# Kernel optimization log

Hardware: AMD Instinct MI355X
Metric: run time of the kernel (lower is better)

## Reference

```python
import jax, jax.numpy as jnp
import numpy as np

HEADS = 16
TOPK = 2048  # dsa_topk


def setup_inputs() -> dict:
    key = jax.random.key(0)
    ks = jax.random.split(key, 9)
    B, Q, KV, C = 2, 2048, 16384, 1024
    w = lambda k: jax.random.normal(k, (C, C), dtype=jnp.float32) * 0.02
    return {
        "hidden_states": jax.random.normal(ks[0], (B, Q, C), dtype=jnp.float32),
        "encoder_hidden_states": jax.random.normal(ks[1], (B, KV, C), dtype=jnp.float32),
        "Wq": w(ks[2]),
        "Wk": w(ks[3]),
        "Wv": w(ks[4]),
        "Wo": w(ks[5]),
        "bo": jnp.zeros((C,), dtype=jnp.float32),
        "Wg": jax.random.normal(ks[6], (C, C), dtype=jnp.float32) * 0.01,  # xavier gain 0.1
        "bg": jnp.full((C,), -1.5, dtype=jnp.float32),  # gate_init_bias
    }


def reference(hidden_states, encoder_hidden_states, Wq, Wk, Wv, Wo, bo, Wg, bg):
    B, Q, C = hidden_states.shape
    H = HEADS
    D = C // H
    scale = 1.0 / jnp.sqrt(jnp.asarray(D, dtype=hidden_states.dtype))

    # projections -> [B, H, S, D]
    q = (hidden_states @ Wq).reshape(B, Q, H, D).transpose(0, 2, 1, 3)
    k = (encoder_hidden_states @ Wk).reshape(B, -1, H, D).transpose(0, 2, 1, 3)
    v = (encoder_hidden_states @ Wv).reshape(B, -1, H, D).transpose(0, 2, 1, 3)

    # _sparse_select: query-summary scored top-k KV gather (kv_len > TOPK here)
    q_summary = q.mean(axis=2)                                   # [B, H, D]
    sel_score = jnp.einsum("bhd,bhkd->bhk", q_summary, k) * scale
    idx = jax.lax.top_k(sel_score, TOPK)[1]                      # [B, H, TOPK]
    k_sel = jnp.take_along_axis(k, idx[..., None], axis=2)       # [B, H, TOPK, D]
    v_sel = jnp.take_along_axis(v, idx[..., None], axis=2)

    # attention over selected KV
    scores = jnp.einsum("bhqd,bhkd->bhqk", q, k_sel) * scale
    probs = jax.nn.softmax(scores.astype(jnp.float32), axis=-1).astype(scores.dtype)
    out = jnp.einsum("bhqk,bhkd->bhqd", probs, v_sel)
    out = out.transpose(0, 2, 1, 3).reshape(B, Q, C)

    # sigmoid gate + output projection (to_out[1] dropout is identity at eval)
    out = out * jax.nn.sigmoid(out @ Wg + bg)
    out = out @ Wo + bo

    # residual_connection=True, rescale_output_factor=1.0
    return out + hidden_states
```

## Files before the change

### kernel.cpp

```cpp
#include <hip/hip_runtime.h>
#include <hip/hip_bf16.h>

typedef unsigned short u16;
typedef __bf16 bf16x8 __attribute__((ext_vector_type(8)));
typedef float f32x4 __attribute__((ext_vector_type(4)));

__device__ __forceinline__ u16 f2bf(float f) {
    union { float f; unsigned int u; } v; v.f = f;
    unsigned int u = v.u;
    unsigned int r = (u + 0x7fffu + ((u >> 16) & 1u)) >> 16;
    return (u16)r;
}
__device__ __forceinline__ float bf2f(u16 b) {
    union { unsigned int u; float f; } v; v.u = ((unsigned int)b) << 16;
    return v.f;
}

__device__ __forceinline__ void glds16(const u16* g, u16* l) {
    __builtin_amdgcn_global_load_lds(
        (__attribute__((address_space(1))) void*)(g),
        (__attribute__((address_space(3))) void*)(l), 16, 0, 0);
}

__global__ __launch_bounds__(256) void cast_bf16_kernel(const float* __restrict__ src,
                                                        u16* __restrict__ dst, int n4) {
    int i = blockIdx.x * 256 + threadIdx.x;
    if (i >= n4) return;
    float4 v = ((const float4*)src)[i];
    ushort4 o;
    o.x = f2bf(v.x); o.y = f2bf(v.y); o.z = f2bf(v.z); o.w = f2bf(v.w);
    ((ushort4*)dst)[i] = o;
}

__global__ __launch_bounds__(256) void transpose_cast_kernel(
    const float* __restrict__ Wq, const float* __restrict__ Wk, const float* __restrict__ Wv,
    const float* __restrict__ Wg, const float* __restrict__ Wo,
    u16* __restrict__ WqT, u16* __restrict__ WkvT, u16* __restrict__ WgT, u16* __restrict__ WoT) {
    __shared__ float tile[32][33];
    const float* src; u16* dst;
    switch (blockIdx.z) {
        case 0: src = Wq; dst = WqT; break;
        case 1: src = Wk; dst = WkvT; break;
        case 2: src = Wv; dst = WkvT + (size_t)1024 * 1024; break;
        case 3: src = Wg; dst = WgT; break;
        default: src = Wo; dst = WoT; break;
    }
    int n0 = blockIdx.x * 32, k0 = blockIdx.y * 32;
    int tx = threadIdx.x, ty = threadIdx.y;
    #pragma unroll
    for (int j = 0; j < 4; j++)
        tile[ty + j * 8][tx] = src[(size_t)(k0 + ty + j * 8) * 1024 + n0 + tx];
    __syncthreads();
    #pragma unroll
    for (int j = 0; j < 4; j++)
        dst[(size_t)(n0 + ty + j * 8) * 1024 + k0 + tx] = f2bf(tile[tx][ty + j * 8]);
}

template <int EPI>
__global__ __launch_bounds__(256) void gemm_bf16(
    const u16* __restrict__ A, const u16* __restrict__ B, int ldc,
    u16* __restrict__ Cbf, const float* __restrict__ bias,
    const u16* __restrict__ mul_src, const float* __restrict__ add_src,
    float* __restrict__ Cf) {
    constexpr int K = 1024;
    const int tid = threadIdx.x;
    const int w = tid >> 6, l = tid & 63;
    const int lr = l & 15, lg = l >> 4;
    const int wr = w >> 1, wc = w & 1;
    const int m0 = blockIdx.y * 128, n0 = blockIdx.x * 128;

    __shared__ u16 As[128 * 64];
    __shared__ u16 Bs[128 * 64];

    const f32x4 fz = {0.f, 0.f, 0.f, 0.f};
    f32x4 acc[4][4];
    #pragma unroll
    for (int i = 0; i < 4; i++)
        #pragma unroll
        for (int j = 0; j < 4; j++) acc[i][j] = fz;

    const int lane_row = l >> 3;
    const int lane_sl  = l & 7;
    const int src_ch   = lane_sl ^ lane_row;
    const u16* Ab = A + (size_t)(m0 + w * 32 + lane_row) * K + src_ch * 8;
    const u16* Bb = B + (size_t)(n0 + w * 32 + lane_row) * K + src_ch * 8;

    for (int kt = 0; kt < K; kt += 64) {
        __syncthreads();
        #pragma unroll
        for (int j = 0; j < 4; j++) {
            glds16(Ab + (size_t)j * 8 * K + kt, As + (w * 32 + j * 8) * 64);
            glds16(Bb + (size_t)j * 8 * K + kt, Bs + (w * 32 + j * 8) * 64);
        }
        __syncthreads();
        #pragma unroll
        for (int kk = 0; kk < 2; kk++) {
            bf16x8 af[4], bfr[4];
            #pragma unroll
            for (int mi = 0; mi < 4; mi++) {
                int row = wr * 64 + mi * 16 + lr;
                int ch = (kk * 4 + lg) ^ (row & 7);
                af[mi] = *(const bf16x8*)(As + row * 64 + ch * 8);
            }
            #pragma unroll
            for (int ni = 0; ni < 4; ni++) {
                int row = wc * 64 + ni * 16 + lr;
                int ch = (kk * 4 + lg) ^ (row & 7);
                bfr[ni] = *(const bf16x8*)(Bs + row * 64 + ch * 8);
            }
            #pragma unroll
            for (int mi = 0; mi < 4; mi++)
                #pragma unroll
                for (int ni = 0; ni < 4; ni++)
                    acc[mi][ni] = __builtin_amdgcn_mfma_f32_16x16x32_bf16(
                        af[mi], bfr[ni], acc[mi][ni], 0, 0, 0);
        }
    }

    #pragma unroll
    for (int mi = 0; mi < 4; mi++) {
        #pragma unroll
        for (int ni = 0; ni < 4; ni++) {
            #pragma unroll
            for (int r = 0; r < 4; r++) {
                int gm = m0 + wr * 64 + mi * 16 + lg * 4 + r;
                int gn = n0 + wc * 64 + ni * 16 + lr;
                float v = acc[mi][ni][r];
                if (EPI == 0) {
                    Cbf[(size_t)gm * ldc + gn] = f2bf(v);
                } else if (EPI == 2) {
                    float g = v + bias[gn];
                    float a = bf2f(mul_src[(size_t)gm * ldc + gn]);
                    float sg = 1.f / (1.f + __expf(-g));
                    Cbf[(size_t)gm * ldc + gn] = f2bf(a * sg);
                } else {
                    Cf[(size_t)gm * ldc + gn] = v + bias[gn] + add_src[(size_t)gm * ldc + gn];
                }
            }
        }
    }
}

__global__ __launch_bounds__(256) void hsum1_kernel(const float* __restrict__ hidden,
                                                    float* __restrict__ part) {
    int b = blockIdx.x, chunk = blockIdx.y;
    int tid = threadIdx.x;
    const float4* src = (const float4*)(hidden + ((size_t)b * 2048 + chunk * 16) * 1024) + tid;
    float4 acc = {0.f, 0.f, 0.f, 0.f};
    #pragma unroll
    for (int r = 0; r < 16; r++) {
        float4 v = src[r * 256];
        acc.x += v.x; acc.y += v.y; acc.z += v.z; acc.w += v.w;
    }
    ((float4*)(part + ((size_t)b * 128 + chunk) * 1024))[tid] = acc;
}

__global__ __launch_bounds__(256) void hsum2_kernel(const float* __restrict__ part,
                                                    float* __restrict__ hm) {
    int b = blockIdx.x, tid = threadIdx.x;
    const float4* src = (const float4*)(part + (size_t)b * 128 * 1024) + tid;
    float4 acc = {0.f, 0.f, 0.f, 0.f};
    for (int c = 0; c < 128; c++) {
        float4 v = src[c * 256];
        acc.x += v.x; acc.y += v.y; acc.z += v.z; acc.w += v.w;
    }
    const float inv = 1.f / 2048.f;
    acc.x *= inv; acc.y *= inv; acc.z *= inv; acc.w *= inv;
    ((float4*)(hm + (size_t)b * 1024))[tid] = acc;
}

__global__ __launch_bounds__(256) void qz_kernel(const float* __restrict__ hm,
                                                 const u16* __restrict__ WqT,
                                                 const u16* __restrict__ WkT,
                                                 u16* __restrict__ z_bf) {
    int bh = blockIdx.x, b = bh >> 4, h = bh & 15;
    int tid = threadIdx.x;
    __shared__ float hm_l[1024];
    __shared__ float qs_l[64];
    __shared__ float red[256];
    ((float4*)hm_l)[tid] = ((const float4*)(hm + (size_t)b * 1024))[tid];
    __syncthreads();
    {
        int d = tid >> 2, q = tid & 3;
        const u16* wq = WqT + (size_t)(h * 64 + d) * 1024 + q * 256;
        float a = 0.f;
        for (int i = 0; i < 256; i += 8) {
            uint4 u = *(const uint4*)(wq + i);
            const u16* p = (const u16*)&u;
            #pragma unroll
            for (int j = 0; j < 8; j++) a += bf2f(p[j]) * hm_l[q * 256 + i + j];
        }
        red[tid] = a;
    }
    __syncthreads();
    if (tid < 64)
        qs_l[tid] = red[tid * 4] + red[tid * 4 + 1] + red[tid * 4 + 2] + red[tid * 4 + 3];
    __syncthreads();
    {
        float z0 = 0.f, z1 = 0.f, z2 = 0.f, z3 = 0.f;
        for (int d = 0; d < 64; d++) {
            float qs = qs_l[d];
            const u16* wk = WkT + (size_t)(h * 64 + d) * 1024 + tid * 4;
            uint2 u = *(const uint2*)wk;
            const u16* p = (const u16*)&u;
            z0 += qs * bf2f(p[0]); z1 += qs * bf2f(p[1]);
            z2 += qs * bf2f(p[2]); z3 += qs * bf2f(p[3]);
        }
        ushort4 o;
        o.x = f2bf(z0); o.y = f2bf(z1); o.z = f2bf(z2); o.w = f2bf(z3);
        *(ushort4*)(z_bf + (size_t)bh * 1024 + tid * 4) = o;
    }
}

__global__ __launch_bounds__(256) void escore_kernel(const float* __restrict__ enc,
                                                     const u16* __restrict__ z_bf,
                                                     u16* __restrict__ ebf,
                                                     float* __restrict__ score) {
    const int b = blockIdx.y, kv0 = blockIdx.x * 128;
    const int tid = threadIdx.x, w = tid >> 6, l = tid & 63;
    const int lr = l & 15, lg = l >> 4;
    __shared__ u16 z_lds[16 * 1024];
    __shared__ u16 e_lds[128 * 64];
    {
        int row = tid >> 4, cg = tid & 15;
        const u16* src = z_bf + (size_t)(b * 16 + row) * 1024 + cg * 64;
        #pragma unroll
        for (int i = 0; i < 8; i++) {
            uint4 u = *(const uint4*)(src + i * 8);
            int ch = cg * 8 + i;
            *(uint4*)(z_lds + row * 1024 + (ch ^ (row & 7)) * 8) = u;
        }
    }
    const int rbase = tid >> 4;
    const int cgrp  = tid & 15;
    const float* ebase = enc + (size_t)(b * 16384 + kv0) * 1024;
    u16* obase = ebf + (size_t)(b * 16384 + kv0) * 1024;

    float4 rv[8];
    auto loadT = [&](int kt) {
        #pragma unroll
        for (int jj = 0; jj < 8; jj++) {
            int row = rbase + jj * 16;
            rv[jj] = *(const float4*)(ebase + (size_t)row * 1024 + kt + cgrp * 4);
        }
    };
    loadT(0);

    const f32x4 fz = {0.f, 0.f, 0.f, 0.f};
    f32x4 acc[2];
    acc[0] = fz; acc[1] = fz;
    __syncthreads();

    for (int kt = 0; kt < 1024; kt += 64) {
        #pragma unroll
        for (int jj = 0; jj < 8; jj++) {
            int row = rbase + jj * 16;
            ushort4 pk;
            pk.x = f2bf(rv[jj].x); pk.y = f2bf(rv[jj].y);
            pk.z = f2bf(rv[jj].z); pk.w = f2bf(rv[jj].w);
            int ch = cgrp >> 1;
            int off = ((ch ^ (row & 7)) * 8) + ((cgrp & 1) * 4);
            *(ushort4*)(e_lds + row * 64 + off) = pk;
            *(ushort4*)(obase + (size_t)row * 1024 + kt + cgrp * 4) = pk;
        }
        __syncthreads();
        if (kt + 64 < 1024) loadT(kt + 64);
        #pragma unroll
        for (int ks = 0; ks < 2; ks++) {
            int chg = (kt >> 3) + ks * 4 + lg;
            bf16x8 af = *(const bf16x8*)(z_lds + lr * 1024 + (chg ^ (lr & 7)) * 8);
            #pragma unroll
            for (int ni = 0; ni < 2; ni++) {
                int row = w * 32 + ni * 16 + lr;
                bf16x8 bf_ = *(const bf16x8*)(e_lds + row * 64 + (((ks * 4 + lg) ^ (lr & 7))) * 8);
                acc[ni] = __builtin_amdgcn_mfma_f32_16x16x32_bf16(af, bf_, acc[ni], 0, 0, 0);
            }
        }
        __syncthreads();
    }
    #pragma unroll
    for (int ni = 0; ni < 2; ni++)
        #pragma unroll
        for (int r = 0; r < 4; r++)
            score[(size_t)(b * 16 + lg * 4 + r) * 16384 + kv0 + w * 32 + ni * 16 + lr] = acc[ni][r];
}

__global__ __launch_bounds__(1024) void select_kernel(const float* __restrict__ score,
                                                      int* __restrict__ sel_idx) {
    const int bh = blockIdx.x;
    const float* sc = score + (size_t)bh * 16384;
    const int tid = threadIdx.x;
    const int grp = tid >> 8;

    __shared__ int hist[4][256];
    __shared__ int total[256];
    __shared__ int bc[4];

    u16 key[16];
    #pragma unroll
    for (int j = 0; j < 16; j++) {
        unsigned int b = __float_as_uint(sc[tid + j * 1024]);
        unsigned int ui = (b & 0x80000000u) ? ~b : (b | 0x80000000u);
        key[j] = (u16)(ui >> 16);
    }

    ((int*)hist)[tid] = 0;
    __syncthreads();
    #pragma unroll
    for (int j = 0; j < 16; j++) atomicAdd(&hist[grp][key[j] >> 8], 1);
    __syncthreads();
    if (tid < 256) total[tid] = hist[0][tid] + hist[1][tid] + hist[2][tid] + hist[3][tid];
    __syncthreads();
    if (tid == 0) {
        int want = 2048, acc = 0;
        for (int dd = 255; dd >= 0; dd--) {
            acc += total[dd];
            if (acc >= want) { bc[0] = dd; bc[1] = want - (acc - total[dd]); break; }
        }
    }
    __syncthreads();
    const int hi = bc[0];
    const int want1 = bc[1];

    ((int*)hist)[tid] = 0;
    __syncthreads();
    #pragma unroll
    for (int j = 0; j < 16; j++)
        if ((key[j] >> 8) == hi) atomicAdd(&hist[grp][key[j] & 0xff], 1);
    __syncthreads();
    if (tid < 256) total[tid] = hist[0][tid] + hist[1][tid] + hist[2][tid] + hist[3][tid];
    __syncthreads();
    if (tid == 0) {
        int want = want1, acc = 0;
        for (int dd = 255; dd >= 0; dd--) {
            acc += total[dd];
            if (acc >= want) { bc[0] = (hi << 8) | dd; bc[1] = want - (acc - total[dd]); break; }
        }
        bc[2] = 0; bc[3] = 0;
    }
    __syncthreads();
    const u16 thr = (u16)bc[0];
    const int n_eq = bc[1];
    const int base_eq = 2048 - n_eq;

    int* out = sel_idx + (size_t)bh * 2048;
    #pragma unroll
    for (int j = 0; j < 16; j++) {
        int i = tid + j * 1024;
        if (key[j] > thr) {
            int p = atomicAdd(&bc[2], 1);
            out[p] = i;
        } else if (key[j] == thr) {
            int p = atomicAdd(&bc[3], 1);
            if (p < n_eq) out[base_eq + p] = i;
        }
    }
}

__global__ __launch_bounds__(256) void selproj_kernel(const u16* __restrict__ ebf,
                                                      const u16* __restrict__ WkvT,
                                                      const int* __restrict__ sel_idx,
                                                      u16* __restrict__ k_sel,
                                                      u16* __restrict__ v_selT) {
    const int bh = blockIdx.y, b = bh >> 4, h = bh & 15;
    const int t0 = blockIdx.x * 128;
    const int tid = threadIdx.x, w = tid >> 6, l = tid & 63;
    const int lr = l & 15, lg = l >> 4;
    const int lane_row = l >> 3, src_ch = (l & 7) ^ lane_row;

    __shared__ u16 e_lds[128 * 64];
    __shared__ u16 w_lds[128 * 64];

    int encrow[4], wrow[4];
    #pragma unroll
    for (int j = 0; j < 4; j++) {
        int t = t0 + w * 32 + j * 8 + lane_row;
        encrow[j] = b * 16384 + sel_idx[(size_t)bh * 2048 + t];
        int r = w * 32 + j * 8 + lane_row;
        wrow[j] = (r < 64) ? (h * 64 + r) : (1024 + h * 64 + (r & 63));
    }

    const f32x4 fz = {0.f, 0.f, 0.f, 0.f};
    f32x4 acc_k[2][4], acc_v[8];
    #pragma unroll
    for (int i = 0; i < 2; i++)
        #pragma unroll
        for (int j = 0; j < 4; j++) acc_k[i][j] = fz;
    #pragma unroll
    for (int i = 0; i < 8; i++) acc_v[i] = fz;

    for (int kt = 0; kt < 1024; kt += 64) {
        __syncthreads();
        #pragma unroll
        for (int j = 0; j < 4; j++) {
            glds16(ebf + (size_t)encrow[j] * 1024 + kt + src_ch * 8, e_lds + (w * 32 + j * 8) * 64);
            glds16(WkvT + (size_t)wrow[j] * 1024 + kt + src_ch * 8, w_lds + (w * 32 + j * 8) * 64);
        }
        __syncthreads();
        #pragma unroll
        for (int ks = 0; ks < 2; ks++) {
            bf16x8 ae[2];
            #pragma unroll
            for (int mi = 0; mi < 2; mi++) {
                int row = w * 32 + mi * 16 + lr;
                ae[mi] = *(const bf16x8*)(e_lds + row * 64 + (((ks * 4 + lg) ^ (row & 7))) * 8);
            }
            bf16x8 aw;
            {
                int row = 64 + w * 16 + lr;
                aw = *(const bf16x8*)(w_lds + row * 64 + (((ks * 4 + lg) ^ (row & 7))) * 8);
            }
            #pragma unroll
            for (int ni = 0; ni < 4; ni++) {
                int row = ni * 16 + lr;
                bf16x8 bw = *(const bf16x8*)(w_lds + row * 64 + (((ks * 4 + lg) ^ (row & 7))) * 8);
                acc_k[0][ni] = __builtin_amdgcn_mfma_f32_16x16x32_bf16(ae[0], bw, acc_k[0][ni], 0, 0, 0);
                acc_k[1][ni] = __builtin_amdgcn_mfma_f32_16x16x32_bf16(ae[1], bw, acc_k[1][ni], 0, 0, 0);
            }
            #pragma unroll
            for (int ni = 0; ni < 8; ni++) {
                int row = ni * 16 + lr;
                bf16x8 be = *(const bf16x8*)(e_lds + row * 64 + (((ks * 4 + lg) ^ (row & 7))) * 8);
                acc_v[ni] = __builtin_amdgcn_mfma_f32_16x16x32_bf16(aw, be, acc_v[ni], 0, 0, 0);
            }
        }
    }

    u16* kb = k_sel + (size_t)bh * 2048 * 64;
    #pragma unroll
    for (int mi = 0; mi < 2; mi++)
        #pragma unroll
        for (int ni = 0; ni < 4; ni++)
            #pragma unroll
            for (int r = 0; r < 4; r++) {
                int t = t0 + w * 32 + mi * 16 + lg * 4 + r;
                int d = ni * 16 + lr;
                kb[(size_t)t * 64 + (((d >> 3) ^ (t & 7)) * 8) + (d & 7)] = f2bf(acc_k[mi][ni][r]);
            }
    u16* vb = v_selT + (size_t)bh * 64 * 2048;
    #pragma unroll
    for (int ni = 0; ni < 8; ni++)
        #pragma unroll
        for (int r = 0; r < 4; r++) {
            int d = w * 16 + lg * 4 + r;
            int t = t0 + ni * 16 + lr;
            int tl = t & 63;
            int kap = (tl & 15) * 4 + (tl >> 4);
            vb[(size_t)d * 2048 + (t & ~63) + (((kap >> 3) ^ (d & 7)) * 8) + (kap & 7)] =
                f2bf(acc_v[ni][r]);
        }
}

__global__ __launch_bounds__(512) void attn_kernel(
    const u16* __restrict__ q_bf, const u16* __restrict__ k_sel,
    const u16* __restrict__ v_selT, u16* __restrict__ attn_out) {
    const int bh = blockIdx.y, b = bh >> 4, h = bh & 15;
    const int q0 = blockIdx.x * 128;
    const int tid = threadIdx.x, w = tid >> 6, l = tid & 63;
    const int lr = l & 15, lg = l >> 4;
    const int lk = lr & 7;
    const float SC = 0.18033688011f;
    const float THR = 11.0f;

    __shared__ u16 k_lds[2][64 * 64];
    __shared__ u16 vt_lds[64 * 64];
    __shared__ u16 p_lds[8][16][68];

    const u16* qb = q_bf + ((size_t)b * 2048 + q0 + w * 16 + lr) * 1024 + h * 64;
    bf16x8 qf0 = *(const bf16x8*)(qb + lg * 8);
    bf16x8 qf1 = *(const bf16x8*)(qb + 32 + lg * 8);

    const f32x4 fz = {0.f, 0.f, 0.f, 0.f};
    f32x4 o[4];
    #pragma unroll
    for (int f = 0; f < 4; f++) o[f] = fz;
    float mm = -1e30f;
    float l_part[4] = {0.f, 0.f, 0.f, 0.f};

    const u16* kb  = k_sel + (size_t)bh * 2048 * 64;
    const u16* vtb = v_selT + (size_t)bh * 64 * 2048;

    auto stageK = [&](int it, int buf) {
        const u16* ksrc = kb + (size_t)(it * 64 + w * 8) * 64 + (size_t)l * 8;
        glds16(ksrc, k_lds[buf] + (w * 8) * 64);
    };
    auto stageV = [&](int it) {
        const u16* vsrc = vtb + (size_t)(w * 8 + (l >> 3)) * 2048 + it * 64 + (l & 7) * 8;
        glds16(vsrc, vt_lds + (w * 8) * 64);
    };

    stageK(0, 0);
    __syncthreads();

    #pragma unroll 1
    for (int it = 0; it < 32; ++it) {
        const int cur = it & 1;
        stageV(it);
        if (it + 1 < 32) stageK(it + 1, cur ^ 1);

        f32x4 s[4];
        #pragma unroll
        for (int c = 0; c < 4; c++) s[c] = fz;
        __builtin_amdgcn_s_setprio(1);
        #pragma unroll
        for (int c = 0; c < 4; c++) {
            const u16* krow = k_lds[cur] + (c * 16 + lr) * 64;
            bf16x8 kf0 = *(const bf16x8*)(krow + (lg ^ lk) * 8);
            s[c] = __builtin_amdgcn_mfma_f32_16x16x32_bf16(qf0, kf0, s[c], 0, 0, 0);
            bf16x8 kf1 = *(const bf16x8*)(krow + (((4 + lg) ^ lk)) * 8);
            s[c] = __builtin_amdgcn_mfma_f32_16x16x32_bf16(qf1, kf1, s[c], 0, 0, 0);
        }
        __builtin_amdgcn_s_setprio(0);

        float mx = s[0][0];
        #pragma unroll
        for (int c = 0; c < 4; c++)
            #pragma unroll
            for (int r = 0; r < 4; r++) mx = fmaxf(mx, s[c][r]);
        mx = fmaxf(mx, __shfl_xor(mx, 1));
        mx = fmaxf(mx, __shfl_xor(mx, 2));
        mx = fmaxf(mx, __shfl_xor(mx, 4));
        mx = fmaxf(mx, __shfl_xor(mx, 8));
        mx = fmaxf(mx, __shfl_xor(mx, 16));
        mx = fmaxf(mx, __shfl_xor(mx, 32));
        mx *= SC;
        if (mx > mm + THR) {
            float al = __builtin_amdgcn_exp2f(mm - mx);
            mm = mx;
            #pragma unroll
            for (int r = 0; r < 4; r++) l_part[r] *= al;
            #pragma unroll
            for (int f = 0; f < 4; f++)
                #pragma unroll
                for (int r = 0; r < 4; r++) o[f][r] *= al;
        }
        #pragma unroll
        for (int r = 0; r < 4; r++) {
            ushort4 pk;
            u16 pb[4];
            #pragma unroll
            for (int c = 0; c < 4; c++) {
                float p = __builtin_amdgcn_exp2f(__builtin_fmaf(s[c][r], SC, -mm));
                l_part[r] += p;
                __bf16 hv = (__bf16)p;
                pb[c] = *(u16*)&hv;
            }
            pk.x = pb[0]; pk.y = pb[1]; pk.z = pb[2]; pk.w = pb[3];
            *(ushort4*)(&p_lds[w][lg * 4 + r][lr * 4]) = pk;
        }

        if (it + 1 < 32) {
            asm volatile("s_waitcnt vmcnt(1)" ::: "memory");
        } else {
            asm volatile("s_waitcnt vmcnt(0)" ::: "memory");
        }
        __builtin_amdgcn_sched_barrier(0);
        __builtin_amdgcn_s_barrier();

        __builtin_amdgcn_s_setprio(1);
        #pragma unroll
        for (int kk = 0; kk < 2; kk++) {
            bf16x8 ap = *(const bf16x8*)(&p_lds[w][lr][kk * 32 + lg * 8]);
            #pragma unroll
            for (int f = 0; f < 4; f++) {
                const u16* vrow = vt_lds + (f * 16 + lr) * 64;
                bf16x8 bv = *(const bf16x8*)(vrow + (((kk * 4 + lg) ^ lk)) * 8);
                o[f] = __builtin_amdgcn_mfma_f32_16x16x32_bf16(ap, bv, o[f], 0, 0, 0);
            }
        }
        __builtin_amdgcn_s_setprio(0);

        __syncthreads();
    }

    float invl[4];
    #pragma unroll
    for (int r = 0; r < 4; r++) {
        float lr_ = l_part[r];
        lr_ += __shfl_xor(lr_, 1);
        lr_ += __shfl_xor(lr_, 2);
        lr_ += __shfl_xor(lr_, 4);
        lr_ += __shfl_xor(lr_, 8);
        invl[r] = 1.f / lr_;
    }
    u16* ob = attn_out + ((size_t)b * 2048 + q0 + w * 16 + lg * 4) * 1024 + h * 64 + lr;
    #pragma unroll
    for (int f = 0; f < 4; f++) {
        #pragma unroll
        for (int r = 0; r < 4; r++) {
            __bf16 hv = (__bf16)(o[f][r] * invl[r]);
            ob[(size_t)r * 1024 + f * 16] = *(u16*)&hv;
        }
    }
}

extern "C" void kernel_launch(void* const* d_in, const int* in_sizes, int n_in,
                              void* d_out, int out_size, void* d_ws, size_t ws_size,
                              hipStream_t stream) {
    const float* hidden = (const float*)d_in[0];
    const float* enc    = (const float*)d_in[1];
    const float* Wq = (const float*)d_in[2];
    const float* Wk = (const float*)d_in[3];
    const float* Wv = (const float*)d_in[4];
    const float* Wo = (const float*)d_in[5];
    const float* bo = (const float*)d_in[6];
    const float* Wg = (const float*)d_in[7];
    const float* bg = (const float*)d_in[8];
    float* out = (float*)d_out;

    char* ws = (char*)d_ws;
    size_t off = 0;
    auto alloc = [&](size_t bytes) -> char* {
        char* p = ws + off;
        off += (bytes + 255) & ~(size_t)255;
        return p;
    };
    u16* hbf   = (u16*)alloc(4096ull * 1024 * 2);
    u16* ebf   = (u16*)alloc(32768ull * 1024 * 2);
    u16* WqT   = (u16*)alloc(1024ull * 1024 * 2);
    u16* WkvT  = (u16*)alloc(2048ull * 1024 * 2);
    u16* WgT   = (u16*)alloc(1024ull * 1024 * 2);
    u16* WoT   = (u16*)alloc(1024ull * 1024 * 2);
    u16* q_bf  = (u16*)alloc(4096ull * 1024 * 2);
    float* hm  = (float*)alloc(2ull * 1024 * 4);
    float* part = (float*)alloc(2ull * 128 * 1024 * 4);
    u16* z_bf  = (u16*)alloc(32ull * 1024 * 2);
    float* scor = (float*)alloc(32ull * 16384 * 4);
    int* sel    = (int*)alloc(32ull * 2048 * 4);
    u16* ksel   = (u16*)alloc(32ull * 2048 * 64 * 2);
    u16* vT     = (u16*)alloc(32ull * 64 * 2048 * 2);
    u16* attn   = (u16*)alloc(4096ull * 1024 * 2);
    u16* gate   = (u16*)alloc(4096ull * 1024 * 2);
    (void)ws_size; (void)in_sizes; (void)n_in; (void)out_size;

    hsum1_kernel<<<dim3(2, 128), 256, 0, stream>>>(hidden, part);
    hsum2_kernel<<<2, 256, 0, stream>>>(part, hm);
    cast_bf16_kernel<<<4096, 256, 0, stream>>>(hidden, hbf, 1048576);
    transpose_cast_kernel<<<dim3(32, 32, 5), dim3(32, 8), 0, stream>>>(
        Wq, Wk, Wv, Wg, Wo, WqT, WkvT, WgT, WoT);

    qz_kernel<<<32, 256, 0, stream>>>(hm, WqT, WkvT, z_bf);
    escore_kernel<<<dim3(128, 2), 256, 0, stream>>>(enc, z_bf, ebf, scor);
    select_kernel<<<32, 1024, 0, stream>>>(scor, sel);
    selproj_kernel<<<dim3(16, 32), 256, 0, stream>>>(ebf, WkvT, sel, ksel, vT);

    gemm_bf16<0><<<dim3(8, 32), 256, 0, stream>>>(hbf, WqT, 1024, q_bf, nullptr, nullptr, nullptr, nullptr);
    attn_kernel<<<dim3(16, 32), 512, 0, stream>>>(q_bf, ksel, vT, attn);

    gemm_bf16<2><<<dim3(8, 32), 256, 0, stream>>>(attn, WgT, 1024, gate, bg, attn, nullptr, nullptr);
    gemm_bf16<3><<<dim3(8, 32), 256, 0, stream>>>(gate, WoT, 1024, nullptr, bo, nullptr, hidden, out);
}
```

Measured before the change: 254.0 us.

## Halve escore tile to 64 rows, read z directly from global

```diff
diff --git a/kernel.cpp b/kernel.cpp
--- a/kernel.cpp
+++ b/kernel.cpp
@@ -216,73 +216,57 @@
                                                      const u16* __restrict__ z_bf,
                                                      u16* __restrict__ ebf,
                                                      float* __restrict__ score) {
-    const int b = blockIdx.y, kv0 = blockIdx.x * 128;
+    const int b = blockIdx.y, kv0 = blockIdx.x * 64;
     const int tid = threadIdx.x, w = tid >> 6, l = tid & 63;
     const int lr = l & 15, lg = l >> 4;
-    __shared__ u16 z_lds[16 * 1024];
-    __shared__ u16 e_lds[128 * 64];
-    {
-        int row = tid >> 4, cg = tid & 15;
-        const u16* src = z_bf + (size_t)(b * 16 + row) * 1024 + cg * 64;
-        #pragma unroll
-        for (int i = 0; i < 8; i++) {
-            uint4 u = *(const uint4*)(src + i * 8);
-            int ch = cg * 8 + i;
-            *(uint4*)(z_lds + row * 1024 + (ch ^ (row & 7)) * 8) = u;
-        }
-    }
-    const int rbase = tid >> 4;
-    const int cgrp  = tid & 15;
+    __shared__ u16 e_lds[64 * 64];
+
+    const int row2 = tid >> 3;
+    const int cgrp = tid & 7;
     const float* ebase = enc + (size_t)(b * 16384 + kv0) * 1024;
     u16* obase = ebf + (size_t)(b * 16384 + kv0) * 1024;
-
-    float4 rv[8];
+    const u16* zb = z_bf + (size_t)b * 16 * 1024;
+
+    float4 rv[2][2];
     auto loadT = [&](int kt) {
         #pragma unroll
-        for (int jj = 0; jj < 8; jj++) {
-            int row = rbase + jj * 16;
-            rv[jj] = *(const float4*)(ebase + (size_t)row * 1024 + kt + cgrp * 4);
+        for (int jj = 0; jj < 2; jj++) {
+            int row = row2 + jj * 32;
+            rv[jj][0] = *(const float4*)(ebase + (size_t)row * 1024 + kt + cgrp * 8);
+            rv[jj][1] = *(const float4*)(ebase + (size_t)row * 1024 + kt + cgrp * 8 + 4);
         }
     };
     loadT(0);
 
     const f32x4 fz = {0.f, 0.f, 0.f, 0.f};
-    f32x4 acc[2];
-    acc[0] = fz; acc[1] = fz;
-    __syncthreads();
+    f32x4 acc = fz;
 
     for (int kt = 0; kt < 1024; kt += 64) {
         #pragma unroll
-        for (int jj = 0; jj < 8; jj++) {
-            int row = rbase + jj * 16;
-            ushort4 pk;
-            pk.x = f2bf(rv[jj].x); pk.y = f2bf(rv[jj].y);
-            pk.z = f2bf(rv[jj].z); pk.w = f2bf(rv[jj].w);
-            int ch = cgrp >> 1;
-            int off = ((ch ^ (row & 7)) * 8) + ((cgrp & 1) * 4);
-            *(ushort4*)(e_lds + row * 64 + off) = pk;
-            *(ushort4*)(obase + (size_t)row * 1024 + kt + cgrp * 4) = pk;
+        for (int jj = 0; jj < 2; jj++) {
+            int row = row2 + jj * 32;
+            union { u16 u[8]; uint4 v; } pk;
+            pk.u[0] = f2bf(rv[jj][0].x); pk.u[1] = f2bf(rv[jj][0].y);
+            pk.u[2] = f2bf(rv[jj][0].z); pk.u[3] = f2bf(rv[jj][0].w);
+            pk.u[4] = f2bf(rv[jj][1].x); pk.u[5] = f2bf(rv[jj][1].y);
+            pk.u[6] = f2bf(rv[jj][1].z); pk.u[7] = f2bf(rv[jj][1].w);
+            *(uint4*)(e_lds + row * 64 + ((cgrp ^ (row & 7)) * 8)) = pk.v;
+            *(uint4*)(obase + (size_t)row * 1024 + kt + cgrp * 8) = pk.v;
         }
         __syncthreads();
         if (kt + 64 < 1024) loadT(kt + 64);
         #pragma unroll
         for (int ks = 0; ks < 2; ks++) {
-            int chg = (kt >> 3) + ks * 4 + lg;
-            bf16x8 af = *(const bf16x8*)(z_lds + lr * 1024 + (chg ^ (lr & 7)) * 8);
-            #pragma unroll
-            for (int ni = 0; ni < 2; ni++) {
-                int row = w * 32 + ni * 16 + lr;
-                bf16x8 bf_ = *(const bf16x8*)(e_lds + row * 64 + (((ks * 4 + lg) ^ (lr & 7))) * 8);
-                acc[ni] = __builtin_amdgcn_mfma_f32_16x16x32_bf16(af, bf_, acc[ni], 0, 0, 0);
-            }
+            bf16x8 af = *(const bf16x8*)(zb + (size_t)lr * 1024 + kt + ks * 32 + lg * 8);
+            int brow = w * 16 + lr;
+            bf16x8 bf_ = *(const bf16x8*)(e_lds + brow * 64 + (((ks * 4 + lg) ^ (brow & 7))) * 8);
+            acc = __builtin_amdgcn_mfma_f32_16x16x32_bf16(af, bf_, acc, 0, 0, 0);
         }
         __syncthreads();
     }
     #pragma unroll
-    for (int ni = 0; ni < 2; ni++)
-        #pragma unroll
-        for (int r = 0; r < 4; r++)
-            score[(size_t)(b * 16 + lg * 4 + r) * 16384 + kv0 + w * 32 + ni * 16 + lr] = acc[ni][r];
+    for (int r = 0; r < 4; r++)
+        score[(size_t)(b * 16 + lg * 4 + r) * 16384 + kv0 + w * 16 + lr] = acc[r];
 }
 
 __global__ __launch_bounds__(1024) void select_kernel(const float* __restrict__ score,
@@ -640,7 +624,7 @@
         Wq, Wk, Wv, Wg, Wo, WqT, WkvT, WgT, WoT);
 
     qz_kernel<<<32, 256, 0, stream>>>(hm, WqT, WkvT, z_bf);
-    escore_kernel<<<dim3(128, 2), 256, 0, stream>>>(enc, z_bf, ebf, scor);
+    escore_kernel<<<dim3(256, 2), 256, 0, stream>>>(enc, z_bf, ebf, scor);
     select_kernel<<<32, 1024, 0, stream>>>(scor, sel);
     selproj_kernel<<<dim3(16, 32), 256, 0, stream>>>(ebf, WkvT, sel, ksel, vT);
 
```

Result: no change. 252.2 us, median of 3 (-0.7%).
